# Kernel tuning notes

Measured on AMD Instinct MI355X. Metric: run time of the kernel, lower is better.

## Reference

```python
import jax, jax.numpy as jnp
import numpy as np

N_NODES = 50000
N_EDGES = 800000
IN_CH = 128
HID = 64
HEADS = 2
OUT_CH = 3
N_GRAPHS = 64
NEG_SLOPE = 0.2


def _gatv2(x, src, dst, Wl, Wr, att, bias, heads, out_ch, concat, n_nodes):
    # GATv2Conv (PyG semantics, eval mode, self-loops already appended)
    xl = (x @ Wl).reshape(n_nodes, heads, out_ch)  # lin_l -> source messages
    xr = (x @ Wr).reshape(n_nodes, heads, out_ch)  # lin_r -> target side
    e = jax.nn.leaky_relu(xl[src] + xr[dst], NEG_SLOPE)          # [E, H, C]
    alpha = jnp.einsum('ehc,hc->eh', e, att)                     # [E, H]
    # segment softmax over incoming edges of each target node
    amax = jax.ops.segment_max(alpha, dst, num_segments=n_nodes)  # [N, H]
    ea = jnp.exp(alpha - amax[dst])
    denom = jax.ops.segment_sum(ea, dst, num_segments=n_nodes)
    alpha = ea / (denom[dst] + 1e-16)
    msg = xl[src] * alpha[..., None]                             # [E, H, C]
    out = jax.ops.segment_sum(msg, dst, num_segments=n_nodes)    # [N, H, C]
    out = out.reshape(n_nodes, heads * out_ch) if concat else out.mean(axis=1)
    return out + bias


def setup_inputs() -> dict:
    key = jax.random.key(0)
    ks = jax.random.split(key, 12)
    x = jax.random.normal(ks[0], (N_NODES, IN_CH), dtype=jnp.float32)
    edge_index = jax.random.randint(ks[1], (2, N_EDGES), 0, N_NODES, dtype=jnp.int64 if jax.config.jax_enable_x64 else jnp.int32)
    batch = jnp.sort(jax.random.randint(ks[2], (N_NODES,), 0, N_GRAPHS))
    s = 0.05
    params = {
        'W1l': jax.random.normal(ks[3], (IN_CH, HEADS * HID), dtype=jnp.float32) * s,
        'W1r': jax.random.normal(ks[4], (IN_CH, HEADS * HID), dtype=jnp.float32) * s,
        'att1': jax.random.normal(ks[5], (HEADS, HID), dtype=jnp.float32) * s,
        'b1': jnp.zeros((HEADS * HID,), dtype=jnp.float32),
        'W2l': jax.random.normal(ks[6], (HEADS * HID, OUT_CH), dtype=jnp.float32) * s,
        'W2r': jax.random.normal(ks[7], (HEADS * HID, OUT_CH), dtype=jnp.float32) * s,
        'att2': jax.random.normal(ks[8], (1, OUT_CH), dtype=jnp.float32) * s,
        'b2': jnp.zeros((OUT_CH,), dtype=jnp.float32),
        'Wr1': jax.random.normal(ks[9], (OUT_CH, 64), dtype=jnp.float32) * s,
        'br1': jnp.zeros((64,), dtype=jnp.float32),
        'Wr2': jax.random.normal(ks[10], (64, 3), dtype=jnp.float32) * s,
        'br2': jnp.zeros((3,), dtype=jnp.float32),
    }
    return {'x': x, 'edge_index': edge_index, 'batch': batch, **params}


def reference(x, edge_index, batch, W1l, W1r, att1, b1, W2l, W2r, att2, b2, Wr1, br1, Wr2, br2):
    n = x.shape[0]
    loops = jnp.arange(n, dtype=edge_index.dtype)
    src = jnp.concatenate([edge_index[0], loops])  # add_self_loops=True
    dst = jnp.concatenate([edge_index[1], loops])
    h = _gatv2(x, src, dst, W1l, W1r, att1, b1, HEADS, HID, True, n)
    h = jax.nn.elu(h)
    h = _gatv2(h, src, dst, W2l, W2r, att2, b2, 1, OUT_CH, False, n)
    # global_mean_pool over graphs
    sums = jax.ops.segment_sum(h, batch, num_segments=N_GRAPHS)
    cnt = jax.ops.segment_sum(jnp.ones((n,), h.dtype), batch, num_segments=N_GRAPHS)
    g = sums / jnp.maximum(cnt, 1.0)[:, None]
    g = jax.nn.relu(g @ Wr1 + br1)
    return g @ Wr2 + br2
```

## Files before the change

kernel.cpp:

```cpp
#include <hip/hip_runtime.h>


#define NGRAPH 64
#define LOG2E 1.4426950408889634f

typedef __attribute__((ext_vector_type(2))) _Float16 hf2;

#define DPP_ROR(C, x) \
  __int_as_float(__builtin_amdgcn_update_dpp(0, __float_as_int(x), (0x120 | C), 0xF, 0xF, false))
#define DPP_QUAD(C, x) \
  __int_as_float(__builtin_amdgcn_update_dpp(0, __float_as_int(x), (C), 0xF, 0xF, false))

__device__ __forceinline__ float rowsum16(float v) {
  v += DPP_ROR(8, v);
  v += DPP_ROR(4, v);
  v += DPP_ROR(2, v);
  v += DPP_ROR(1, v);
  return v;
}

__device__ __forceinline__ unsigned bf16rne(float f) {
  unsigned u = __float_as_uint(f);
  return (u + 0x7FFFu + ((u >> 16) & 1u)) >> 16;
}

__device__ __forceinline__ unsigned short f16u(float f) {
  union { _Float16 h; unsigned short u; } v;
  v.h = (_Float16)f;
  return v.u;
}

__device__ __forceinline__ hf2 as_hf2(unsigned u) {
  union { unsigned u; hf2 h; } v;
  v.u = u;
  return v.h;
}

typedef __attribute__((ext_vector_type(8))) short bf16x8;
typedef __attribute__((ext_vector_type(4))) float f32x4;

__global__ void k_deg(const int* __restrict__ ei, int E, int Et,
                      int* __restrict__ deg, int* __restrict__ rank) {
  int e = blockIdx.x * blockDim.x + threadIdx.x;
  if (e >= Et) return;
  int d = (e < E) ? ei[E + e] : (e - E);
  rank[e] = atomicAdd(&deg[d], 1);
}

__global__ __launch_bounds__(256) void k_scan_part(const int* __restrict__ deg,
                                                   int* __restrict__ bsum, int n) {
  __shared__ int sd[256];
  int t = threadIdx.x;
  int i = blockIdx.x * 1024 + t * 4;
  int s = 0;
  if (i + 4 <= n) {
    int4 d = *(const int4*)&deg[i];
    s = d.x + d.y + d.z + d.w;
  } else {
    for (int j = i; j < min(i + 4, n); ++j) s += deg[j];
  }
  sd[t] = s;
  __syncthreads();
  for (int off = 128; off; off >>= 1) {
    if (t < off) sd[t] += sd[t + off];
    __syncthreads();
  }
  if (t == 0) bsum[blockIdx.x] = sd[0];
}

__global__ __launch_bounds__(64) void k_scan_top(int* __restrict__ bsum, int nb) {
  __shared__ int s[64];
  int t = threadIdx.x;
  s[t] = (t < nb) ? bsum[t] : 0;
  __syncthreads();
  int acc = 0;
  for (int j = 0; j < t; ++j) acc += s[j];
  if (t < nb) bsum[t] = acc;
}

__global__ __launch_bounds__(256) void k_scan_write(const int* __restrict__ deg,
                                                    const int* __restrict__ bsum,
                                                    int* __restrict__ row_ptr, int n) {
  __shared__ int sd[256];
  int t = threadIdx.x;
  int i = blockIdx.x * 1024 + t * 4;
  int4 d = make_int4(0, 0, 0, 0);
  bool full = (i + 4 <= n);
  if (full) d = *(const int4*)&deg[i];
  else {
    if (i + 0 < n) d.x = deg[i + 0];
    if (i + 1 < n) d.y = deg[i + 1];
    if (i + 2 < n) d.z = deg[i + 2];
    if (i + 3 < n) d.w = deg[i + 3];
  }
  int s = d.x + d.y + d.z + d.w;
  sd[t] = s;
  __syncthreads();
  for (int off = 1; off < 256; off <<= 1) {
    int v = (t >= off) ? sd[t - off] : 0;
    __syncthreads();
    sd[t] += v;
    __syncthreads();
  }
  int ex = sd[t] - s + bsum[blockIdx.x];
  int4 r;
  r.x = ex;
  r.y = ex + d.x;
  r.z = r.y + d.y;
  r.w = r.z + d.z;
  if (full) {
    *(int4*)&row_ptr[i] = r;
    if (i + 4 == n) row_ptr[n] = r.w + d.w;
  } else if (i < n) {
    int run = ex;
    int vals[4] = {d.x, d.y, d.z, d.w};
    for (int j = 0; j < 4 && i + j < n; ++j) {
      row_ptr[i + j] = run;
      run += vals[j];
    }
    if (i <= n && i + 4 > n) row_ptr[n] = run;
  }
}

__global__ void k_fill(const int* __restrict__ ei, int E, int Et,
                       const int* __restrict__ row_ptr,
                       const int* __restrict__ rank,
                       int* __restrict__ csr_src) {
  int e = blockIdx.x * blockDim.x + threadIdx.x;
  if (e >= Et) return;
  int s, d;
  if (e < E) { s = ei[e]; d = ei[E + e]; }
  else       { s = e - E; d = s; }
  csr_src[row_ptr[d] + rank[e]] = s;
}

__global__ __launch_bounds__(256) void k_cvt(const float* __restrict__ x,
                                             const float* __restrict__ W1l,
                                             const float* __restrict__ W1r,
                                             unsigned short* __restrict__ xhp,
                                             unsigned short* __restrict__ xlp,
                                             unsigned short* __restrict__ whp,
                                             unsigned short* __restrict__ wlp,
                                             int n, int RB) {
  int t = threadIdx.x;
  int kc = t >> 6;
  int l = t & 63;
  int lr = l & 15;
  int k0 = kc * 32 + (l >> 4) * 8;
  int b = blockIdx.x;
  float f[8];
  if (b < RB) {
    int row = b * 16 + lr;
    if (row < n) {
      float4 a = *(const float4*)&x[(size_t)row * 128 + k0];
      float4 c = *(const float4*)&x[(size_t)row * 128 + k0 + 4];
      f[0] = a.x; f[1] = a.y; f[2] = a.z; f[3] = a.w;
      f[4] = c.x; f[5] = c.y; f[6] = c.z; f[7] = c.w;
    } else {
#pragma unroll
      for (int j = 0; j < 8; ++j) f[j] = 0.f;
    }
  } else {
    int col = (b - RB) * 16 + lr;
#pragma unroll
    for (int j = 0; j < 8; ++j)
      f[j] = (col < 128) ? W1l[(size_t)(k0 + j) * 128 + col]
                         : W1r[(size_t)(k0 + j) * 128 + (col - 128)];
  }
  unsigned hv[8], lv[8];
#pragma unroll
  for (int j = 0; j < 8; ++j) {
    hv[j] = bf16rne(f[j]);
    float r = f[j] - __uint_as_float(hv[j] << 16);
    lv[j] = bf16rne(r);
  }
  uint4 ph, pl;
  ph.x = hv[0] | (hv[1] << 16); ph.y = hv[2] | (hv[3] << 16);
  ph.z = hv[4] | (hv[5] << 16); ph.w = hv[6] | (hv[7] << 16);
  pl.x = lv[0] | (lv[1] << 16); pl.y = lv[2] | (lv[3] << 16);
  pl.z = lv[4] | (lv[5] << 16); pl.w = lv[6] | (lv[7] << 16);
  if (b < RB) {
    size_t slot = (((size_t)b * 4 + kc) * 64 + l) * 8;
    *(uint4*)&xhp[slot] = ph;
    *(uint4*)&xlp[slot] = pl;
  } else {
    size_t slot = (((size_t)(b - RB) * 4 + kc) * 64 + l) * 8;
    *(uint4*)&whp[slot] = ph;
    *(uint4*)&wlp[slot] = pl;
  }
}

__global__ __launch_bounds__(256) void k_gmfma(const unsigned short* __restrict__ xhp,
                                               const unsigned short* __restrict__ xlp,
                                               const unsigned short* __restrict__ whp,
                                               const unsigned short* __restrict__ wlp,
                                               unsigned short* __restrict__ outl,
                                               unsigned short* __restrict__ outr, int n) {
  int w = threadIdx.x >> 6;
  int lane = threadIdx.x & 63;
  int lr = lane & 15;
  int r0 = blockIdx.x * 32;
  int rb0 = blockIdx.x * 2;

  f32x4 acc[2][4] = {};

#pragma unroll
  for (int kc = 0; kc < 4; ++kc) {
    bf16x8 ah[2], al[2], bh[4], bl[4];
#pragma unroll
    for (int m = 0; m < 2; ++m) {
      size_t slot = (((size_t)(rb0 + m) * 4 + kc) * 64 + lane) * 8;
      ah[m] = *(const bf16x8*)&xhp[slot];
      al[m] = *(const bf16x8*)&xlp[slot];
    }
#pragma unroll
    for (int f = 0; f < 4; ++f) {
      size_t slot = (((size_t)(w * 4 + f) * 4 + kc) * 64 + lane) * 8;
      bh[f] = *(const bf16x8*)&whp[slot];
      bl[f] = *(const bf16x8*)&wlp[slot];
    }
#pragma unroll
    for (int m = 0; m < 2; ++m)
#pragma unroll
      for (int f = 0; f < 4; ++f) {
        acc[m][f] = __builtin_amdgcn_mfma_f32_16x16x32_bf16(ah[m], bh[f], acc[m][f], 0, 0, 0);
        acc[m][f] = __builtin_amdgcn_mfma_f32_16x16x32_bf16(ah[m], bl[f], acc[m][f], 0, 0, 0);
        acc[m][f] = __builtin_amdgcn_mfma_f32_16x16x32_bf16(al[m], bh[f], acc[m][f], 0, 0, 0);
      }
  }

  int rbase = (lane >> 4) * 4;
  unsigned short* dst = (w < 2) ? outl : outr;
  int cb = (w & 1) * 64;
#pragma unroll
  for (int m = 0; m < 2; ++m)
#pragma unroll
    for (int f = 0; f < 4; ++f) {
      int col = cb + f * 16 + lr;
#pragma unroll
      for (int i = 0; i < 4; ++i) {
        int row = r0 + m * 16 + rbase + i;
        if (row < n)
          dst[(size_t)row * 128 + col] = f16u(acc[m][f][i]);
      }
    }
}

__global__ __launch_bounds__(256) void k_fused1(const unsigned short* __restrict__ xl,
                                                const unsigned short* __restrict__ xr,
                                                const int* __restrict__ row_ptr,
                                                const int* __restrict__ csr_src,
                                                const float* __restrict__ att1,
                                                const float* __restrict__ b1,
                                                const float* __restrict__ W2l,
                                                const float* __restrict__ W2r,
                                                float* __restrict__ xl2,
                                                float* __restrict__ xr2, int n) {
  int wid  = (blockIdx.x * 256 + threadIdx.x) >> 6;
  int lane = threadIdx.x & 63;
  int sub  = lane & 31;
  int node = min(wid * 2 + (lane >> 5), n - 1);
  int ch = sub * 4;
  const char* xlb = (const char*)xl;
  unsigned chb = (unsigned)sub * 8u;

  uint2 xrq = *(const uint2*)&xr[(size_t)node * 128 + ch];
  hf2 xr01 = as_hf2(xrq.x), xr23 = as_hf2(xrq.y);
  float4 atv = *(const float4*)&att1[ch];
  hf2 at01, at23;
  at01.x = (_Float16)(atv.x * LOG2E); at01.y = (_Float16)(atv.y * LOG2E);
  at23.x = (_Float16)(atv.z * LOG2E); at23.y = (_Float16)(atv.w * LOG2E);
  hf2 k02; k02.x = (_Float16)0.2f; k02.y = (_Float16)0.2f;

  int s0 = row_ptr[node];
  int deg = row_ptr[node + 1] - s0;
  int odeg = __shfl_xor(deg, 32);
  int mindeg = min(deg, odeg);
  int maxdeg = max(deg, odeg);
  const int* sp = csr_src + s0;

  float m = -1e30f, l = 0.f;
  float4 acc = make_float4(0.f, 0.f, 0.f, 0.f);

#define EDGE(p, x0, x1, x2, x3, q)                                      \
    { hf2 v01 = as_hf2(q.x), v23 = as_hf2(q.y);                         \
      hf2 t01 = v01 + xr01, t23 = v23 + xr23;                           \
      hf2 l01 = __builtin_elementwise_max(t01, t01 * k02);              \
      hf2 l23 = __builtin_elementwise_max(t23, t23 * k02);              \
      p = __builtin_amdgcn_fdot2(l23, at23,                             \
            __builtin_amdgcn_fdot2(l01, at01, 0.f, false), false);      \
      x0 = (float)l01.x;             \
      x0 = (float)v01.x; x1 = (float)v01.y;                             \
      x2 = (float)v23.x; x3 = (float)v23.y; }

#define BODY(CLAMPED)                                                   \
  {                                                                     \
    int sA, sB, sC, sD;                                                 \
    if (CLAMPED) {                                                      \
      int dm1 = deg - 1;                                                \
      sA = sp[min(e + 0, dm1)];                                         \
      sB = sp[min(e + 1, dm1)];                                         \
      sC = sp[min(e + 2, dm1)];                                         \
      sD = sp[min(e + 3, dm1)];                                         \
    } else {                                                            \
      sA = sp[e + 0]; sB = sp[e + 1]; sC = sp[e + 2]; sD = sp[e + 3];   \
    }                                                                   \
    uint2 qa = *(const uint2*)(xlb + (((unsigned)sA << 8) + chb));      \
    uint2 qb = *(const uint2*)(xlb + (((unsigned)sB << 8) + chb));      \
    uint2 qc = *(const uint2*)(xlb + (((unsigned)sC << 8) + chb));      \
    uint2 qd = *(const uint2*)(xlb + (((unsigned)sD << 8) + chb));      \
    float pa, pb, pc, pd;                                               \
    float xa0, xa1, xa2, xa3, xb0, xb1, xb2, xb3;                       \
    float xc0, xc1, xc2, xc3, xd0, xd1, xd2, xd3;                       \
    EDGE(pa, xa0, xa1, xa2, xa3, qa)                                    \
    EDGE(pb, xb0, xb1, xb2, xb3, qb)                                    \
    EDGE(pc, xc0, xc1, xc2, xc3, qc)                                    \
    EDGE(pd, xd0, xd1, xd2, xd3, qd)                                    \
    pa = rowsum16(pa);                                                  \
    pb = rowsum16(pb);                                                  \
    pc = rowsum16(pc);                                                  \
    pd = rowsum16(pd);                                                  \
    if (CLAMPED) {                                                      \
      pa = (e + 0 < deg) ? pa : -1e30f;                                 \
      pb = (e + 1 < deg) ? pb : -1e30f;                                 \
      pc = (e + 2 < deg) ? pc : -1e30f;                                 \
      pd = (e + 3 < deg) ? pd : -1e30f;                                 \
    }                                                                   \
    float mn = fmaxf(m, fmaxf(fmaxf(pa, pb), fmaxf(pc, pd)));           \
    float sc = exp2f(m - mn);                                           \
    float wa = exp2f(pa - mn);                                          \
    float wb = exp2f(pb - mn);                                          \
    float wc = exp2f(pc - mn);                                          \
    float wd = exp2f(pd - mn);                                          \
    acc.x = fmaf(wd, xd0, fmaf(wc, xc0, fmaf(wb, xb0, fmaf(wa, xa0, acc.x * sc)))); \
    acc.y = fmaf(wd, xd1, fmaf(wc, xc1, fmaf(wb, xb1, fmaf(wa, xa1, acc.y * sc)))); \
    acc.z = fmaf(wd, xd2, fmaf(wc, xc2, fmaf(wb, xb2, fmaf(wa, xa2, acc.z * sc)))); \
    acc.w = fmaf(wd, xd3, fmaf(wc, xc3, fmaf(wb, xb3, fmaf(wa, xa3, acc.w * sc)))); \
    l = fmaf(l, sc, wa + wb + wc + wd);                                 \
    m = mn;                                                             \
  }

  int e = 0;
  for (; e + 4 <= mindeg; e += 4) BODY(false)
  for (; e < maxdeg; e += 4) BODY(true)
#undef BODY
#undef EDGE

  float inv = 1.f / (l + 1e-16f);
  float4 b1v = *(const float4*)&b1[ch];
  float4 h;
  h.x = acc.x * inv + b1v.x; h.x = h.x > 0.f ? h.x : expm1f(h.x);
  h.y = acc.y * inv + b1v.y; h.y = h.y > 0.f ? h.y : expm1f(h.y);
  h.z = acc.z * inv + b1v.z; h.z = h.z > 0.f ? h.z : expm1f(h.z);
  h.w = acc.w * inv + b1v.w; h.w = h.w > 0.f ? h.w : expm1f(h.w);

  float4 u0 = *(const float4*)&W2l[ch * 3 + 0];
  float4 u1 = *(const float4*)&W2l[ch * 3 + 4];
  float4 u2 = *(const float4*)&W2l[ch * 3 + 8];
  float al0 = fmaf(h.w, u2.y, fmaf(h.z, u1.z, fmaf(h.y, u0.w, h.x * u0.x)));
  float al1 = fmaf(h.w, u2.z, fmaf(h.z, u1.w, fmaf(h.y, u1.x, h.x * u0.y)));
  float al2 = fmaf(h.w, u2.w, fmaf(h.z, u2.x, fmaf(h.y, u1.y, h.x * u0.z)));
  float4 v0 = *(const float4*)&W2r[ch * 3 + 0];
  float4 v1 = *(const float4*)&W2r[ch * 3 + 4];
  float4 v2 = *(const float4*)&W2r[ch * 3 + 8];
  float ar0 = fmaf(h.w, v2.y, fmaf(h.z, v1.z, fmaf(h.y, v0.w, h.x * v0.x)));
  float ar1 = fmaf(h.w, v2.z, fmaf(h.z, v1.w, fmaf(h.y, v1.x, h.x * v0.y)));
  float ar2 = fmaf(h.w, v2.w, fmaf(h.z, v2.x, fmaf(h.y, v1.y, h.x * v0.z)));
#pragma unroll
  for (int off = 1; off < 32; off <<= 1) {
    al0 += __shfl_xor(al0, off); al1 += __shfl_xor(al1, off);
    al2 += __shfl_xor(al2, off); ar0 += __shfl_xor(ar0, off);
    ar1 += __shfl_xor(ar1, off); ar2 += __shfl_xor(ar2, off);
  }
  if (sub == 0 && wid * 2 + (lane >> 5) < n) {
    *(float4*)&xl2[node * 4] = make_float4(al0, al1, al2, 0.f);
    *(float4*)&xr2[node * 4] = make_float4(ar0, ar1, ar2, 0.f);
  }
}

__global__ __launch_bounds__(256) void k_fused2(const float* __restrict__ xl2,
                                                const float* __restrict__ xr2,
                                                const int* __restrict__ row_ptr,
                                                const int* __restrict__ csr_src,
                                                const float* __restrict__ att2,
                                                const float* __restrict__ b2,
                                                const int* __restrict__ batch,
                                                float* __restrict__ gsum,
                                                float* __restrict__ gcnt, int n) {
  __shared__ float ls[NGRAPH * 3];
  __shared__ float lc[NGRAPH];
  int t = threadIdx.x;
  for (int i = t; i < NGRAPH * 3; i += 256) ls[i] = 0.f;
  for (int i = t; i < NGRAPH; i += 256) lc[i] = 0.f;
  __syncthreads();

  int node = (blockIdx.x * 256 + t) >> 2;
  int lane = t & 3;
  if (node < n) {
    float4 xrv = *(const float4*)&xr2[node * 4];
    float c0 = att2[0] * LOG2E, c1 = att2[1] * LOG2E, c2 = att2[2] * LOG2E;
    int s0 = row_ptr[node], s1 = row_ptr[node + 1];
    float m = -1e30f, l = 0.f, a0 = 0.f, a1 = 0.f, a2 = 0.f;
    for (int slot = s0 + lane; slot < s1; slot += 4) {
      int s = csr_src[slot];
      float4 xlv = *(const float4*)&xl2[s * 4];
      float t0 = xlv.x + xrv.x; t0 = fmaxf(t0, 0.2f * t0);
      float t1 = xlv.y + xrv.y; t1 = fmaxf(t1, 0.2f * t1);
      float t2 = xlv.z + xrv.z; t2 = fmaxf(t2, 0.2f * t2);
      float p = fmaf(t2, c2, fmaf(t1, c1, t0 * c0));
      float mn = fmaxf(m, p);
      float sc = exp2f(m - mn);
      float w  = exp2f(p - mn);
      a0 = a0 * sc + w * xlv.x;
      a1 = a1 * sc + w * xlv.y;
      a2 = a2 * sc + w * xlv.z;
      l = l * sc + w;
      m = mn;
    }
#define MERGEQ(C)                                                       \
    {                                                                   \
      float m2 = DPP_QUAD(C, m);                                        \
      float l2 = DPP_QUAD(C, l);                                        \
      float b0 = DPP_QUAD(C, a0);                                       \
      float b1v = DPP_QUAD(C, a1);                                      \
      float b2v = DPP_QUAD(C, a2);                                      \
      float mn = fmaxf(m, m2);                                          \
      float sA = exp2f(m - mn);                                         \
      float sB = exp2f(m2 - mn);                                        \
      a0 = a0 * sA + b0 * sB;                                           \
      a1 = a1 * sA + b1v * sB;                                          \
      a2 = a2 * sA + b2v * sB;                                          \
      l = l * sA + l2 * sB;                                             \
      m = mn;                                                           \
    }
    MERGEQ(0x39) MERGEQ(0x4E)
#undef MERGEQ
    if (lane == 0) {
      float inv = 1.f / (l + 1e-16f);
      float o0 = a0 * inv + b2[0];
      float o1 = a1 * inv + b2[1];
      float o2 = a2 * inv + b2[2];
      int b = batch[node];
      atomicAdd(&ls[b * 3 + 0], o0);
      atomicAdd(&ls[b * 3 + 1], o1);
      atomicAdd(&ls[b * 3 + 2], o2);
      atomicAdd(&lc[b], 1.f);
    }
  }
  __syncthreads();
  for (int i = t; i < NGRAPH * 3; i += 256)
    if (ls[i] != 0.f) atomicAdd(&gsum[i], ls[i]);
  for (int i = t; i < NGRAPH; i += 256)
    if (lc[i] != 0.f) atomicAdd(&gcnt[i], lc[i]);
}

__global__ __launch_bounds__(64) void k_mlp(const float* __restrict__ gsum,
                                            const float* __restrict__ gcnt,
                                            const float* __restrict__ Wr1,
                                            const float* __restrict__ br1,
                                            const float* __restrict__ Wr2,
                                            const float* __restrict__ br2,
                                            float* __restrict__ out) {
  int t = threadIdx.x;
  if (t >= NGRAPH) return;
  float cnt = fmaxf(gcnt[t], 1.f);
  float g0 = gsum[t * 3 + 0] / cnt;
  float g1 = gsum[t * 3 + 1] / cnt;
  float g2 = gsum[t * 3 + 2] / cnt;
  float o0 = br2[0], o1 = br2[1], o2 = br2[2];
  for (int j = 0; j < 64; ++j) {
    float hj = g0 * Wr1[j] + g1 * Wr1[64 + j] + g2 * Wr1[128 + j] + br1[j];
    hj = fmaxf(hj, 0.f);
    o0 = fmaf(hj, Wr2[j * 3 + 0], o0);
    o1 = fmaf(hj, Wr2[j * 3 + 1], o1);
    o2 = fmaf(hj, Wr2[j * 3 + 2], o2);
  }
  out[t * 3 + 0] = o0;
  out[t * 3 + 1] = o1;
  out[t * 3 + 2] = o2;
}

extern "C" void kernel_launch(void* const* d_in, const int* in_sizes, int n_in,
                              void* d_out, int out_size, void* d_ws, size_t ws_size,
                              hipStream_t stream) {
  const float* x    = (const float*)d_in[0];
  const int*   ei   = (const int*)d_in[1];
  const int*   batch= (const int*)d_in[2];
  const float* W1l  = (const float*)d_in[3];
  const float* W1r  = (const float*)d_in[4];
  const float* att1 = (const float*)d_in[5];
  const float* b1   = (const float*)d_in[6];
  const float* W2l  = (const float*)d_in[7];
  const float* W2r  = (const float*)d_in[8];
  const float* att2 = (const float*)d_in[9];
  const float* b2   = (const float*)d_in[10];
  const float* Wr1  = (const float*)d_in[11];
  const float* br1  = (const float*)d_in[12];
  const float* Wr2  = (const float*)d_in[13];
  const float* br2  = (const float*)d_in[14];
  float* out = (float*)d_out;

  const int N  = in_sizes[0] / 128;
  const int E  = in_sizes[1] / 2;
  const int Et = E + N;
  const int NB = (N + 1023) / 1024;
  const int NB32 = (N + 31) / 32;
  const int RB = NB32 * 2;

  char* p = (char*)d_ws;
  auto alloc = [&](size_t bytes) -> char* {
    char* r = p;
    p += (bytes + 255) & ~(size_t)255;
    return r;
  };
  unsigned short* xl1 = (unsigned short*)alloc((size_t)N * 128 * 2);
  unsigned short* xr1 = (unsigned short*)alloc((size_t)N * 128 * 2);
  int*      row_ptr= (int*)alloc((size_t)(N + 1) * 4);
  int*      csr_src= (int*)alloc((size_t)Et * 4);
  int*      rank   = (int*)alloc((size_t)Et * 4);
  int*      bsum   = (int*)alloc(64 * 4);
  char*     z0     = p;
  int*      deg    = (int*)alloc((size_t)N * 4);
  float*    gsum   = (float*)alloc(NGRAPH * 3 * 4);
  float*    gcnt   = (float*)alloc(NGRAPH * 4);
  size_t    zbytes = (size_t)(p - z0);
  float*    xl2    = (float*)alloc((size_t)N * 4 * 4);
  float*    xr2    = (float*)alloc((size_t)N * 4 * 4);
  unsigned short* xhp = (unsigned short*)alloc((size_t)RB * 2048 * 2);
  unsigned short* xlp = (unsigned short*)alloc((size_t)RB * 2048 * 2);
  unsigned short* whp = (unsigned short*)alloc((size_t)16 * 2048 * 2);
  unsigned short* wlp = (unsigned short*)alloc((size_t)16 * 2048 * 2);

  hipMemsetAsync(z0, 0, zbytes, stream);
  hipLaunchKernelGGL(k_deg, dim3((Et + 255) / 256), dim3(256), 0, stream,
                     ei, E, Et, deg, rank);
  hipLaunchKernelGGL(k_scan_part, dim3(NB), dim3(256), 0, stream, deg, bsum, N);
  hipLaunchKernelGGL(k_scan_top, dim3(1), dim3(64), 0, stream, bsum, NB);
  hipLaunchKernelGGL(k_scan_write, dim3(NB), dim3(256), 0, stream,
                     deg, bsum, row_ptr, N);
  hipLaunchKernelGGL(k_fill, dim3((Et + 255) / 256), dim3(256), 0, stream,
                     ei, E, Et, row_ptr, rank, csr_src);
  hipLaunchKernelGGL(k_cvt, dim3(RB + 16), dim3(256), 0, stream,
                     x, W1l, W1r, xhp, xlp, whp, wlp, N, RB);
  hipLaunchKernelGGL(k_gmfma, dim3(NB32), dim3(256), 0, stream,
                     xhp, xlp, whp, wlp, xl1, xr1, N);
  int waves1 = (N + 1) / 2;
  hipLaunchKernelGGL(k_fused1, dim3((waves1 * 64 + 255) / 256), dim3(256), 0, stream,
                     xl1, xr1, row_ptr, csr_src, att1, b1, W2l, W2r, xl2, xr2, N);
  hipLaunchKernelGGL(k_fused2, dim3((N * 4 + 255) / 256), dim3(256), 0, stream,
                     xl2, xr2, row_ptr, csr_src, att2, b2, batch, gsum, gcnt, N);
  hipLaunchKernelGGL(k_mlp, dim3(1), dim3(64), 0, stream,
                     gsum, gcnt, Wr1, br1, Wr2, br2, out);
}
```

Before: 245.4 us.

## Fuse x bf16 hi/lo split into GEMM kernel via LDS staging

The conversion of x into packed bf16 high/low pairs moves out of the separate conversion kernel and into the MFMA GEMM kernel. Each block converts its 32 rows and stages them in shared memory before the MFMA loop, and only the weight conversion stays as a small kernel. This removes a global write and re-read of the two packed x buffers (about 25 MB of traffic) and their workspace. In exchange the GEMM kernel adds LDS use and a block barrier. A dead duplicate assignment is also removed.

```diff
diff --git a/kernel.cpp b/kernel.cpp
--- a/kernel.cpp
+++ b/kernel.cpp
@@ -134,39 +134,22 @@
   csr_src[row_ptr[d] + rank[e]] = s;
 }
 
-__global__ __launch_bounds__(256) void k_cvt(const float* __restrict__ x,
-                                             const float* __restrict__ W1l,
-                                             const float* __restrict__ W1r,
-                                             unsigned short* __restrict__ xhp,
-                                             unsigned short* __restrict__ xlp,
-                                             unsigned short* __restrict__ whp,
-                                             unsigned short* __restrict__ wlp,
-                                             int n, int RB) {
+__global__ __launch_bounds__(256) void k_cvtw(const float* __restrict__ W1l,
+                                              const float* __restrict__ W1r,
+                                              unsigned short* __restrict__ whp,
+                                              unsigned short* __restrict__ wlp) {
   int t = threadIdx.x;
   int kc = t >> 6;
   int l = t & 63;
   int lr = l & 15;
-  int k0 = kc * 32 + (l >> 4) * 8;
+  int k0 = kc * 32 + ((l >> 4) << 3);
   int b = blockIdx.x;
+  int col = b * 16 + lr;
   float f[8];
-  if (b < RB) {
-    int row = b * 16 + lr;
-    if (row < n) {
-      float4 a = *(const float4*)&x[(size_t)row * 128 + k0];
-      float4 c = *(const float4*)&x[(size_t)row * 128 + k0 + 4];
-      f[0] = a.x; f[1] = a.y; f[2] = a.z; f[3] = a.w;
-      f[4] = c.x; f[5] = c.y; f[6] = c.z; f[7] = c.w;
-    } else {
-#pragma unroll
-      for (int j = 0; j < 8; ++j) f[j] = 0.f;
-    }
-  } else {
-    int col = (b - RB) * 16 + lr;
-#pragma unroll
-    for (int j = 0; j < 8; ++j)
-      f[j] = (col < 128) ? W1l[(size_t)(k0 + j) * 128 + col]
-                         : W1r[(size_t)(k0 + j) * 128 + (col - 128)];
-  }
+#pragma unroll
+  for (int j = 0; j < 8; ++j)
+    f[j] = (col < 128) ? W1l[(size_t)(k0 + j) * 128 + col]
+                       : W1r[(size_t)(k0 + j) * 128 + (col - 128)];
   unsigned hv[8], lv[8];
 #pragma unroll
   for (int j = 0; j < 8; ++j) {
@@ -179,28 +162,59 @@
   ph.z = hv[4] | (hv[5] << 16); ph.w = hv[6] | (hv[7] << 16);
   pl.x = lv[0] | (lv[1] << 16); pl.y = lv[2] | (lv[3] << 16);
   pl.z = lv[4] | (lv[5] << 16); pl.w = lv[6] | (lv[7] << 16);
-  if (b < RB) {
-    size_t slot = (((size_t)b * 4 + kc) * 64 + l) * 8;
-    *(uint4*)&xhp[slot] = ph;
-    *(uint4*)&xlp[slot] = pl;
-  } else {
-    size_t slot = (((size_t)(b - RB) * 4 + kc) * 64 + l) * 8;
-    *(uint4*)&whp[slot] = ph;
-    *(uint4*)&wlp[slot] = pl;
-  }
-}
-
-__global__ __launch_bounds__(256) void k_gmfma(const unsigned short* __restrict__ xhp,
-                                               const unsigned short* __restrict__ xlp,
+  size_t slot = (((size_t)b * 4 + kc) * 64 + l) * 8;
+  *(uint4*)&whp[slot] = ph;
+  *(uint4*)&wlp[slot] = pl;
+}
+
+__global__ __launch_bounds__(256) void k_gmfma(const float* __restrict__ x,
                                                const unsigned short* __restrict__ whp,
                                                const unsigned short* __restrict__ wlp,
                                                unsigned short* __restrict__ outl,
                                                unsigned short* __restrict__ outr, int n) {
-  int w = threadIdx.x >> 6;
-  int lane = threadIdx.x & 63;
+  __shared__ __align__(16) unsigned short xh_lds[2 * 4 * 64 * 8];
+  __shared__ __align__(16) unsigned short xl_lds[2 * 4 * 64 * 8];
+  int t = threadIdx.x;
+  int skc = t >> 6;
+  int sl = t & 63;
+  int slr = sl & 15;
+  int sk0 = skc * 32 + ((sl >> 4) << 3);
+  int r0 = blockIdx.x * 32;
+
+#pragma unroll
+  for (int rb = 0; rb < 2; ++rb) {
+    int row = r0 + rb * 16 + slr;
+    float f[8];
+    if (row < n) {
+      float4 a = *(const float4*)&x[(size_t)row * 128 + sk0];
+      float4 c = *(const float4*)&x[(size_t)row * 128 + sk0 + 4];
+      f[0] = a.x; f[1] = a.y; f[2] = a.z; f[3] = a.w;
+      f[4] = c.x; f[5] = c.y; f[6] = c.z; f[7] = c.w;
+    } else {
+#pragma unroll
+      for (int j = 0; j < 8; ++j) f[j] = 0.f;
+    }
+    unsigned hv[8], lv[8];
+#pragma unroll
+    for (int j = 0; j < 8; ++j) {
+      hv[j] = bf16rne(f[j]);
+      float r = f[j] - __uint_as_float(hv[j] << 16);
+      lv[j] = bf16rne(r);
+    }
+    uint4 ph, pl;
+    ph.x = hv[0] | (hv[1] << 16); ph.y = hv[2] | (hv[3] << 16);
+    ph.z = hv[4] | (hv[5] << 16); ph.w = hv[6] | (hv[7] << 16);
+    pl.x = lv[0] | (lv[1] << 16); pl.y = lv[2] | (lv[3] << 16);
+    pl.z = lv[4] | (lv[5] << 16); pl.w = lv[6] | (lv[7] << 16);
+    int slot = ((rb * 4 + skc) * 64 + sl) * 8;
+    *(uint4*)&xh_lds[slot] = ph;
+    *(uint4*)&xl_lds[slot] = pl;
+  }
+  __syncthreads();
+
+  int w = t >> 6;
+  int lane = t & 63;
   int lr = lane & 15;
-  int r0 = blockIdx.x * 32;
-  int rb0 = blockIdx.x * 2;
 
   f32x4 acc[2][4] = {};
 
@@ -209,9 +223,9 @@
     bf16x8 ah[2], al[2], bh[4], bl[4];
 #pragma unroll
     for (int m = 0; m < 2; ++m) {
-      size_t slot = (((size_t)(rb0 + m) * 4 + kc) * 64 + lane) * 8;
-      ah[m] = *(const bf16x8*)&xhp[slot];
-      al[m] = *(const bf16x8*)&xlp[slot];
+      int slot = ((m * 4 + kc) * 64 + lane) * 8;
+      ah[m] = *(const bf16x8*)&xh_lds[slot];
+      al[m] = *(const bf16x8*)&xl_lds[slot];
     }
 #pragma unroll
     for (int f = 0; f < 4; ++f) {
@@ -289,7 +303,6 @@
       hf2 l23 = __builtin_elementwise_max(t23, t23 * k02);              \
       p = __builtin_amdgcn_fdot2(l23, at23,                             \
             __builtin_amdgcn_fdot2(l01, at01, 0.f, false), false);      \
-      x0 = (float)l01.x;             \
       x0 = (float)v01.x; x1 = (float)v01.y;                             \
       x2 = (float)v23.x; x3 = (float)v23.y; }
 
@@ -505,7 +518,6 @@
   const int Et = E + N;
   const int NB = (N + 1023) / 1024;
   const int NB32 = (N + 31) / 32;
-  const int RB = NB32 * 2;
 
   char* p = (char*)d_ws;
   auto alloc = [&](size_t bytes) -> char* {
@@ -526,8 +538,6 @@
   size_t    zbytes = (size_t)(p - z0);
   float*    xl2    = (float*)alloc((size_t)N * 4 * 4);
   float*    xr2    = (float*)alloc((size_t)N * 4 * 4);
-  unsigned short* xhp = (unsigned short*)alloc((size_t)RB * 2048 * 2);
-  unsigned short* xlp = (unsigned short*)alloc((size_t)RB * 2048 * 2);
   unsigned short* whp = (unsigned short*)alloc((size_t)16 * 2048 * 2);
   unsigned short* wlp = (unsigned short*)alloc((size_t)16 * 2048 * 2);
 
@@ -540,10 +550,10 @@
                      deg, bsum, row_ptr, N);
   hipLaunchKernelGGL(k_fill, dim3((Et + 255) / 256), dim3(256), 0, stream,
                      ei, E, Et, row_ptr, rank, csr_src);
-  hipLaunchKernelGGL(k_cvt, dim3(RB + 16), dim3(256), 0, stream,
-                     x, W1l, W1r, xhp, xlp, whp, wlp, N, RB);
+  hipLaunchKernelGGL(k_cvtw, dim3(16), dim3(256), 0, stream,
+                     W1l, W1r, whp, wlp);
   hipLaunchKernelGGL(k_gmfma, dim3(NB32), dim3(256), 0, stream,
-                     xhp, xlp, whp, wlp, xl1, xr1, N);
+                     x, whp, wlp, xl1, xr1, N);
   int waves1 = (N + 1) / 2;
   hipLaunchKernelGGL(k_fused1, dim3((waves1 * 64 + 255) / 256), dim3(256), 0, stream,
                      xl1, xr1, row_ptr, csr_src, att1, b1, W2l, W2r, xl2, xr2, N);
```

Result: faster. 238.9 us (-2.6%).
